# Kernel optimization log

Measured on AMD Instinct MI355X. Metric: run time of the kernel, lower is better.

Reference implementation:

```python
import jax, jax.numpy as jnp
import numpy as np

B, C, L = 32, 8, 2048
K, S = 512, 64  # num_shapelets, shapelets_size


def setup_inputs() -> dict:
    key = jax.random.key(0)
    k1, k2 = jax.random.split(key)
    x = jax.random.normal(k1, (B, C, L), dtype=jnp.float32)
    shapelets = jax.random.normal(k2, (C, K, S), dtype=jnp.float32)
    return {"x": x, "shapelets": shapelets}


def reference(x, shapelets):
    # x: [B, C, L]; shapelets: [C, K, S]
    s = shapelets.shape[-1]
    n_dims = x.shape[1]
    W = x.shape[2] - s + 1  # number of sliding windows
    # unfold(2, S, 1): gather overlapping windows -> [B, C, W, S]
    idx = jnp.arange(W)[:, None] + jnp.arange(s)[None, :]
    xw = x[:, :, idx]
    # L2-normalize windows along window length (clamp min like torch)
    xw = xw / jnp.maximum(jnp.linalg.norm(xw, axis=-1, keepdims=True), 1e-8)
    # L2-normalize shapelets along length
    sn = shapelets / jnp.maximum(jnp.linalg.norm(shapelets, axis=-1, keepdims=True), 1e-8)
    # matmul [B,C,W,S] @ [C,S,K] then sum over C, fused into one einsum -> [B, W, K]
    sim = jnp.einsum('bcws,cks->bwk', xw, sn) / n_dims
    sim = jax.nn.relu(sim)
    # max over window positions -> [B, K]; keep the singleton channel dim like torch ([B,1,K])
    out = jnp.max(sim, axis=1)
    return out[:, None, :]
```

## Files before the change

### kernel.cpp

```cpp
#include <hip/hip_runtime.h>


#define B_ 32
#define C_ 8
#define L_ 2048
#define K_ 512
#define S_ 64
#define W_ 1985
#define TW 128

typedef _Float16 f16x8 __attribute__((ext_vector_type(8)));
typedef float f32x16 __attribute__((ext_vector_type(16)));
typedef float f32x4u __attribute__((ext_vector_type(4), aligned(4)));

__global__ __launch_bounds__(256)
void prep_k(const float* __restrict__ x, const float* __restrict__ sh,
            _Float16* __restrict__ Bp, float* __restrict__ invn,
            float* __restrict__ out) {
    __shared__ float xr[L_];
    const int tid = threadIdx.x;
    const int blk = blockIdx.x;

    if (blk < 128) {
        const int sb   = blk * 4 + (tid >> 6);
        const int c    = sb >> 6;
        const int kq   = (sb >> 4) & 3;
        const int nt   = sb & 15;
        const int lane = tid & 63;
        const int half = lane >> 5;
        const int q    = nt * 32 + (lane & 31);

        const float4* sp = (const float4*)(sh + (size_t)(c * K_ + q) * S_);
        float ss = 0.f;
        #pragma unroll
        for (int i = 0; i < 8; ++i) {
            float4 v = sp[half * 8 + i];
            ss += v.x * v.x + v.y * v.y + v.z * v.z + v.w * v.w;
        }
        ss += __shfl_xor(ss, 32);
        float inv = 1.f / fmaxf(sqrtf(ss), 1e-8f);

        float4 u0 = sp[kq * 4 + half * 2];
        float4 u1 = sp[kq * 4 + half * 2 + 1];
        f16x8 o;
        o[0] = (_Float16)(u0.x * inv); o[1] = (_Float16)(u0.y * inv);
        o[2] = (_Float16)(u0.z * inv); o[3] = (_Float16)(u0.w * inv);
        o[4] = (_Float16)(u1.x * inv); o[5] = (_Float16)(u1.y * inv);
        o[6] = (_Float16)(u1.z * inv); o[7] = (_Float16)(u1.w * inv);
        ((f16x8*)Bp)[((c * 4 + kq) * 16 + nt) * 64 + lane] = o;
    } else {
        const int r = blk - 128;
        const float* xp = x + (size_t)r * L_;
        for (int i = tid; i < L_ / 4; i += 256)
            ((float4*)xr)[i] = ((const float4*)xp)[i];
        __syncthreads();

        float* ivp = invn + (size_t)r * L_;
        const int w0 = tid * 8;
        float ss = 0.f;
        if (w0 < W_) {
            #pragma unroll
            for (int j = 0; j < S_; ++j) { float v = xr[w0 + j]; ss += v * v; }
        }
        #pragma unroll
        for (int u = 0; u < 8; ++u) {
            int w = w0 + u;
            float o = 0.f;
            if (u > 0 && w < W_)
                ss += xr[w + 63] * xr[w + 63] - xr[w - 1] * xr[w - 1];
            if (w < W_) o = 0.125f / fmaxf(sqrtf(ss), 1e-8f);
            if (w < L_) ivp[w] = o;
        }
        if (r < 64) out[r * 256 + tid] = 0.f;
    }
}

__global__ __launch_bounds__(256, 2)
void mcs_k(const float* __restrict__ x, const _Float16* __restrict__ Bp,
           const float* __restrict__ invn, float* __restrict__ out) {
    const int wt  = blockIdx.x;
    const int ng  = blockIdx.y;
    const int b   = blockIdx.z;
    const int tid = threadIdx.x;
    const int lane = tid & 63;
    const int wv   = tid >> 6;
    const int mg   = wv >> 1;
    const int nw   = wv & 1;

    const int l31 = lane & 31;
    const int lh  = lane >> 5;
    const int Wb  = wt * TW + mg * 64;

    const float* xbase  = x    + (size_t)(b * C_) * L_;
    const float* ivbase = invn + (size_t)(b * C_) * L_;
    const f16x8* Bq     = (const f16x8*)Bp;
    const int coloff    = (ng * 8 + nw * 4) * 64 + lane;

    f16x8  Bbuf[3][4];
    f32x4u Abuf[2][4];
    float  iv0b[2], iv1b[2];

    auto issueB = [&](int s, int slot) {
        const int c = s >> 2, ks = s & 3;
        const f16x8* bb = Bq + ((c * 4 + ks) * 16) * 64 + coloff;
        #pragma unroll
        for (int nt = 0; nt < 4; ++nt) Bbuf[slot][nt] = bb[nt * 64];
    };
    auto issueA = [&](int s, int slot) {
        const int c = s >> 2, ks = s & 3;
        const float* xr = xbase + c * L_;
        #pragma unroll
        for (int mt = 0; mt < 2; ++mt) {
            int p  = Wb + mt * 32 + l31 + ks * 16 + lh * 8;
            int pc = p <= L_ - 8 ? p : L_ - 8;
            Abuf[slot][mt * 2]     = *(const f32x4u*)(xr + pc);
            Abuf[slot][mt * 2 + 1] = *(const f32x4u*)(xr + pc + 4);
        }
    };

    iv0b[0] = ivbase[Wb + l31];
    iv1b[0] = ivbase[Wb + 32 + l31];
    issueB(0, 0);
    issueA(0, 0);
    issueB(1, 1);

    f32x16 acc[2][4];
    #pragma unroll
    for (int mt = 0; mt < 2; ++mt)
        #pragma unroll
        for (int nt = 0; nt < 4; ++nt)
            #pragma unroll
            for (int r = 0; r < 16; ++r) acc[mt][nt][r] = 0.f;

    #pragma unroll
    for (int s = 0; s < 32; ++s) {
        const int c = s >> 2, ks = s & 3;
        if (s + 2 < 32) issueB(s + 2, (s + 2) % 3);
        if (s + 1 < 32) issueA(s + 1, (s + 1) & 1);
        if (ks == 0 && c + 1 < C_) {
            const float* ivr = ivbase + (c + 1) * L_;
            iv0b[(c + 1) & 1] = ivr[Wb + l31];
            iv1b[(c + 1) & 1] = ivr[Wb + 32 + l31];
        }
        const float iv0 = iv0b[c & 1], iv1 = iv1b[c & 1];
        f16x8 af0, af1;
        {
            f32x4u v0 = Abuf[s & 1][0], v1 = Abuf[s & 1][1];
            af0[0] = (_Float16)(v0[0] * iv0); af0[1] = (_Float16)(v0[1] * iv0);
            af0[2] = (_Float16)(v0[2] * iv0); af0[3] = (_Float16)(v0[3] * iv0);
            af0[4] = (_Float16)(v1[0] * iv0); af0[5] = (_Float16)(v1[1] * iv0);
            af0[6] = (_Float16)(v1[2] * iv0); af0[7] = (_Float16)(v1[3] * iv0);
            f32x4u w0 = Abuf[s & 1][2], w1 = Abuf[s & 1][3];
            af1[0] = (_Float16)(w0[0] * iv1); af1[1] = (_Float16)(w0[1] * iv1);
            af1[2] = (_Float16)(w0[2] * iv1); af1[3] = (_Float16)(w0[3] * iv1);
            af1[4] = (_Float16)(w1[0] * iv1); af1[5] = (_Float16)(w1[1] * iv1);
            af1[6] = (_Float16)(w1[2] * iv1); af1[7] = (_Float16)(w1[3] * iv1);
        }
        #pragma unroll
        for (int nt = 0; nt < 4; ++nt) {
            acc[0][nt] = __builtin_amdgcn_mfma_f32_32x32x16_f16(
                af0, Bbuf[s % 3][nt], acc[0][nt], 0, 0, 0);
            acc[1][nt] = __builtin_amdgcn_mfma_f32_32x32x16_f16(
                af1, Bbuf[s % 3][nt], acc[1][nt], 0, 0, 0);
        }
    }

    #pragma unroll
    for (int nt = 0; nt < 4; ++nt) {
        float m = 0.f;
        #pragma unroll
        for (int mt = 0; mt < 2; ++mt)
            #pragma unroll
            for (int r = 0; r < 16; ++r)
                m = fmaxf(m, acc[mt][nt][r]);
        m = fmaxf(m, __shfl_xor(m, 32));
        if (lane < 32)
            atomicMax((unsigned int*)(out + b * K_ + ng * 256 + nw * 128 + nt * 32 + l31),
                      __float_as_uint(m));
    }
}

extern "C" void kernel_launch(void* const* d_in, const int* in_sizes, int n_in,
                              void* d_out, int out_size, void* d_ws, size_t ws_size,
                              hipStream_t stream) {
    const float* x  = (const float*)d_in[0];
    const float* sh = (const float*)d_in[1];
    float* out = (float*)d_out;
    _Float16* Bp  = (_Float16*)d_ws;
    float* invn   = (float*)((char*)d_ws + (size_t)K_ * 512 * sizeof(_Float16));

    prep_k<<<dim3(384), dim3(256), 0, stream>>>(x, sh, Bp, invn, out);
    mcs_k<<<dim3(16, 2, B_), dim3(256), 0, stream>>>(x, Bp, invn, out);
}
```

Before: 103.7 us.

## Pre-convert x to fp16 with a shifted copy and halve N per block

The prep kernel now writes fp16 copies of x, including a one-element-shifted copy so odd lanes get 4-byte-aligned 16-byte loads, and stores the inverse window norms as fp16. The main kernel loads A fragments directly as fp16 and scales them with a packed fp16 multiply instead of doing per-element fp32 multiply and convert. Each block now covers 128 shapelets instead of 256, which doubles the grid and raises the occupancy hint to 4 blocks per CU. The cost is extra prep writes and fp16 rounding of the norm scale before the multiply.

Measured after the change: 115.8 us. 1.12x slower.

```diff
diff --git a/kernel.cpp b/kernel.cpp
--- a/kernel.cpp
+++ b/kernel.cpp
@@ -10,12 +10,13 @@
 #define TW 128
 
 typedef _Float16 f16x8 __attribute__((ext_vector_type(8)));
+typedef _Float16 f16x8u __attribute__((ext_vector_type(8), aligned(4)));
 typedef float f32x16 __attribute__((ext_vector_type(16)));
-typedef float f32x4u __attribute__((ext_vector_type(4), aligned(4)));
 
 __global__ __launch_bounds__(256)
 void prep_k(const float* __restrict__ x, const float* __restrict__ sh,
-            _Float16* __restrict__ Bp, float* __restrict__ invn,
+            _Float16* __restrict__ Bp, _Float16* __restrict__ xh0,
+            _Float16* __restrict__ xh1, _Float16* __restrict__ invh,
             float* __restrict__ out) {
     __shared__ float xr[L_];
     const int tid = threadIdx.x;
@@ -55,7 +56,20 @@
             ((float4*)xr)[i] = ((const float4*)xp)[i];
         __syncthreads();
 
-        float* ivp = invn + (size_t)r * L_;
+        {
+            const int i = tid * 8;
+            f16x8 a, bsh;
+            #pragma unroll
+            for (int j = 0; j < 8; ++j) {
+                a[j]   = (_Float16)xr[i + j];
+                int n  = i + j + 1;
+                bsh[j] = (_Float16)(n < L_ ? xr[n] : 0.f);
+            }
+            *(f16x8*)(xh0 + (size_t)r * L_ + i) = a;
+            *(f16x8*)(xh1 + (size_t)r * L_ + i) = bsh;
+        }
+
+        _Float16* ivp = invh + (size_t)r * L_;
         const int w0 = tid * 8;
         float ss = 0.f;
         if (w0 < W_) {
@@ -69,15 +83,16 @@
             if (u > 0 && w < W_)
                 ss += xr[w + 63] * xr[w + 63] - xr[w - 1] * xr[w - 1];
             if (w < W_) o = 0.125f / fmaxf(sqrtf(ss), 1e-8f);
-            if (w < L_) ivp[w] = o;
+            if (w < L_) ivp[w] = (_Float16)o;
         }
         if (r < 64) out[r * 256 + tid] = 0.f;
     }
 }
 
-__global__ __launch_bounds__(256, 2)
-void mcs_k(const float* __restrict__ x, const _Float16* __restrict__ Bp,
-           const float* __restrict__ invn, float* __restrict__ out) {
+__global__ __launch_bounds__(256, 4)
+void mcs_k(const _Float16* __restrict__ Bp, const _Float16* __restrict__ xh0,
+           const _Float16* __restrict__ xh1, const _Float16* __restrict__ invh,
+           float* __restrict__ out) {
     const int wt  = blockIdx.x;
     const int ng  = blockIdx.y;
     const int b   = blockIdx.z;
@@ -90,45 +105,45 @@
     const int l31 = lane & 31;
     const int lh  = lane >> 5;
     const int Wb  = wt * TW + mg * 64;
-
-    const float* xbase  = x    + (size_t)(b * C_) * L_;
-    const float* ivbase = invn + (size_t)(b * C_) * L_;
+    const int par = l31 & 1;
+
+    const _Float16* xb  = (par ? xh1 - 1 : xh0) + (size_t)(b * C_) * L_;
+    const _Float16* ivb = invh + (size_t)(b * C_) * L_;
     const f16x8* Bq     = (const f16x8*)Bp;
-    const int coloff    = (ng * 8 + nw * 4) * 64 + lane;
-
-    f16x8  Bbuf[3][4];
-    f32x4u Abuf[2][4];
-    float  iv0b[2], iv1b[2];
+    const int coloff    = (ng * 4 + nw * 2) * 64 + lane;
+
+    f16x8  Bbuf[3][2];
+    f16x8u Abuf[2][2];
+    _Float16 ivr[2][2];
 
     auto issueB = [&](int s, int slot) {
         const int c = s >> 2, ks = s & 3;
         const f16x8* bb = Bq + ((c * 4 + ks) * 16) * 64 + coloff;
-        #pragma unroll
-        for (int nt = 0; nt < 4; ++nt) Bbuf[slot][nt] = bb[nt * 64];
+        Bbuf[slot][0] = bb[0];
+        Bbuf[slot][1] = bb[64];
     };
     auto issueA = [&](int s, int slot) {
         const int c = s >> 2, ks = s & 3;
-        const float* xr = xbase + c * L_;
+        const _Float16* xr = xb + c * L_;
         #pragma unroll
         for (int mt = 0; mt < 2; ++mt) {
             int p  = Wb + mt * 32 + l31 + ks * 16 + lh * 8;
             int pc = p <= L_ - 8 ? p : L_ - 8;
-            Abuf[slot][mt * 2]     = *(const f32x4u*)(xr + pc);
-            Abuf[slot][mt * 2 + 1] = *(const f32x4u*)(xr + pc + 4);
+            Abuf[slot][mt] = *(const f16x8u*)(xr + pc);
         }
     };
 
-    iv0b[0] = ivbase[Wb + l31];
-    iv1b[0] = ivbase[Wb + 32 + l31];
+    ivr[0][0] = ivb[Wb + l31];
+    ivr[0][1] = ivb[Wb + 32 + l31];
     issueB(0, 0);
     issueA(0, 0);
     issueB(1, 1);
 
-    f32x16 acc[2][4];
+    f32x16 acc[2][2];
     #pragma unroll
     for (int mt = 0; mt < 2; ++mt)
         #pragma unroll
-        for (int nt = 0; nt < 4; ++nt)
+        for (int nt = 0; nt < 2; ++nt)
             #pragma unroll
             for (int r = 0; r < 16; ++r) acc[mt][nt][r] = 0.f;
 
@@ -138,26 +153,15 @@
         if (s + 2 < 32) issueB(s + 2, (s + 2) % 3);
         if (s + 1 < 32) issueA(s + 1, (s + 1) & 1);
         if (ks == 0 && c + 1 < C_) {
-            const float* ivr = ivbase + (c + 1) * L_;
-            iv0b[(c + 1) & 1] = ivr[Wb + l31];
-            iv1b[(c + 1) & 1] = ivr[Wb + 32 + l31];
-        }
-        const float iv0 = iv0b[c & 1], iv1 = iv1b[c & 1];
-        f16x8 af0, af1;
-        {
-            f32x4u v0 = Abuf[s & 1][0], v1 = Abuf[s & 1][1];
-            af0[0] = (_Float16)(v0[0] * iv0); af0[1] = (_Float16)(v0[1] * iv0);
-            af0[2] = (_Float16)(v0[2] * iv0); af0[3] = (_Float16)(v0[3] * iv0);
-            af0[4] = (_Float16)(v1[0] * iv0); af0[5] = (_Float16)(v1[1] * iv0);
-            af0[6] = (_Float16)(v1[2] * iv0); af0[7] = (_Float16)(v1[3] * iv0);
-            f32x4u w0 = Abuf[s & 1][2], w1 = Abuf[s & 1][3];
-            af1[0] = (_Float16)(w0[0] * iv1); af1[1] = (_Float16)(w0[1] * iv1);
-            af1[2] = (_Float16)(w0[2] * iv1); af1[3] = (_Float16)(w0[3] * iv1);
-            af1[4] = (_Float16)(w1[0] * iv1); af1[5] = (_Float16)(w1[1] * iv1);
-            af1[6] = (_Float16)(w1[2] * iv1); af1[7] = (_Float16)(w1[3] * iv1);
-        }
-        #pragma unroll
-        for (int nt = 0; nt < 4; ++nt) {
+            const _Float16* ivn = ivb + (c + 1) * L_;
+            ivr[(c + 1) & 1][0] = ivn[Wb + l31];
+            ivr[(c + 1) & 1][1] = ivn[Wb + 32 + l31];
+        }
+        f16x8 af0 = (f16x8)Abuf[s & 1][0] * ivr[c & 1][0];
+        f16x8 af1 = (f16x8)Abuf[s & 1][1] * ivr[c & 1][1];
+
+        #pragma unroll
+        for (int nt = 0; nt < 2; ++nt) {
             acc[0][nt] = __builtin_amdgcn_mfma_f32_32x32x16_f16(
                 af0, Bbuf[s % 3][nt], acc[0][nt], 0, 0, 0);
             acc[1][nt] = __builtin_amdgcn_mfma_f32_32x32x16_f16(
@@ -166,7 +170,7 @@
     }
 
     #pragma unroll
-    for (int nt = 0; nt < 4; ++nt) {
+    for (int nt = 0; nt < 2; ++nt) {
         float m = 0.f;
         #pragma unroll
         for (int mt = 0; mt < 2; ++mt)
@@ -175,7 +179,7 @@
                 m = fmaxf(m, acc[mt][nt][r]);
         m = fmaxf(m, __shfl_xor(m, 32));
         if (lane < 32)
-            atomicMax((unsigned int*)(out + b * K_ + ng * 256 + nw * 128 + nt * 32 + l31),
+            atomicMax((unsigned int*)(out + b * K_ + ng * 128 + nw * 64 + nt * 32 + l31),
                       __float_as_uint(m));
     }
 }
@@ -186,9 +190,13 @@
     const float* x  = (const float*)d_in[0];
     const float* sh = (const float*)d_in[1];
     float* out = (float*)d_out;
-    _Float16* Bp  = (_Float16*)d_ws;
-    float* invn   = (float*)((char*)d_ws + (size_t)K_ * 512 * sizeof(_Float16));
-
-    prep_k<<<dim3(384), dim3(256), 0, stream>>>(x, sh, Bp, invn, out);
-    mcs_k<<<dim3(16, 2, B_), dim3(256), 0, stream>>>(x, Bp, invn, out);
+
+    char* ws = (char*)d_ws;
+    _Float16* Bp   = (_Float16*)ws;
+    _Float16* xh0  = (_Float16*)(ws + (512 << 10));
+    _Float16* xh1  = (_Float16*)(ws + (512 << 10) + (1 << 20));
+    _Float16* invh = (_Float16*)(ws + (512 << 10) + (2 << 20));
+
+    prep_k<<<dim3(384), dim3(256), 0, stream>>>(x, sh, Bp, xh0, xh1, invh, out);
+    mcs_k<<<dim3(16, 4, B_), dim3(256), 0, stream>>>(Bp, xh0, xh1, invh, out);
 }
```
